# Kernel tuning notes

Measured on AMD Instinct MI355X. Metric: run time of the kernel, lower is better.

Reference implementation:

```python
import jax, jax.numpy as jnp
import numpy as np

IMAGE_SIZE = 256
DET = int(IMAGE_SIZE * 2 ** 0.5 + 0.5)  # 362 detector bins (diagonal coverage)
US = 4
N_ACQ = 45                     # acquired views: 0,4,...,176 degrees
N_FULL = (N_ACQ - 1) * US + 1  # 177 full (upsampled) views


def setup_inputs() -> dict:
    key = jax.random.key(0)
    k1, k2 = jax.random.split(key)
    x_source = jax.random.normal(k1, (2, 1, IMAGE_SIZE, IMAGE_SIZE), jnp.float32)
    s_target = jax.random.normal(k2, (2, 1, DET, N_ACQ), jnp.float32)
    theta_acq = np.arange(0, 180, 4, dtype=np.float64)  # 45 acquired angles
    segs = [np.linspace(theta_acq[i], theta_acq[i + 1], US + 1)[:-1] for i in range(N_ACQ - 1)]
    theta_full = np.concatenate(segs + [theta_acq[-1:]]).astype(np.float32)  # [177]
    acq_idx = (np.arange(N_ACQ) * US).astype(np.int32)  # positions of acquired angles in theta_full
    return {"x_source": x_source, "s_target": s_target,
            "thetas_deg": jnp.asarray(theta_full), "acq_idx": jnp.asarray(acq_idx)}


def bilinear_gather(img, xs, ys):
    # img: [B,C,H,W]; xs, ys: pixel coords [A,det,det]; zero outside the image.
    H, W = img.shape[-2], img.shape[-1]
    x0 = jnp.floor(xs); y0 = jnp.floor(ys)
    wx = xs - x0; wy = ys - y0
    x0i = x0.astype(jnp.int32); y0i = y0.astype(jnp.int32)

    def get(yi, xi):
        valid = (xi >= 0) & (xi < W) & (yi >= 0) & (yi < H)
        v = img[:, :, jnp.clip(yi, 0, H - 1), jnp.clip(xi, 0, W - 1)]  # [B,C,A,det,det]
        return jnp.where(valid, v, 0.0)

    return (get(y0i, x0i) * (1 - wy) * (1 - wx)
            + get(y0i, x0i + 1) * (1 - wy) * wx
            + get(y0i + 1, x0i) * wy * (1 - wx)
            + get(y0i + 1, x0i + 1) * wy * wx)


def radon(x, thetas_rad, det):
    # Ray-sum projection: sino[theta, t] = sum_s image(t*cos - s*sin, t*sin + s*cos)
    B, C, H, W = x.shape
    t = jnp.arange(det, dtype=x.dtype) - (det - 1) / 2.0  # centered detector/ray coord
    cos = jnp.cos(thetas_rad)[:, None, None]
    sin = jnp.sin(thetas_rad)[:, None, None]
    T = t[None, :, None]; S = t[None, None, :]
    xs = T * cos - S * sin + (W - 1) / 2.0  # [A,det,det]
    ys = T * sin + S * cos + (H - 1) / 2.0
    return bilinear_gather(x, xs, ys).sum(-1)  # [B,C,A,det]


def ramp_filter(size):
    # skimage/pytorch_radon style ramp built from its real-space kernel
    n = np.concatenate([np.arange(1, size // 2 + 1, 2), np.arange(size // 2 - 1, 0, -2)])
    f = np.zeros(size)
    f[0] = 0.25
    f[1::2] = -1.0 / (np.pi * n) ** 2
    return jnp.asarray(2 * np.real(np.fft.fft(f)), dtype=jnp.float32)


def fbp(sino, thetas_rad, image_size):
    # Filtered back-projection. sino: [B,C,det,A]
    B, C, det, A = sino.shape
    pad = max(64, int(2 ** np.ceil(np.log2(2 * det))))
    filt = ramp_filter(pad)  # [pad]
    sp = jnp.pad(sino, ((0, 0), (0, 0), (0, pad - det), (0, 0)))
    sf = jnp.fft.ifft(jnp.fft.fft(sp, axis=2) * filt[None, None, :, None], axis=2).real
    sf = jnp.transpose(sf[:, :, :det, :], (0, 1, 3, 2)).astype(sino.dtype)  # [B,C,A,det]
    g = jnp.arange(image_size, dtype=sino.dtype) - (image_size - 1) / 2.0
    cos = jnp.cos(thetas_rad); sin = jnp.sin(thetas_rad)
    # detector coordinate hit by each pixel, per angle: t = x*cos + y*sin
    t = (cos[:, None, None] * g[None, None, :]
         + sin[:, None, None] * g[None, :, None] + (det - 1) / 2.0)  # [A,H,W]
    t = t.reshape(A, -1)
    t0 = jnp.floor(t)
    w = t - t0
    t0i = t0.astype(jnp.int32)
    aidx = jnp.arange(A)[:, None]

    def samp(ti):
        valid = (ti >= 0) & (ti < det)
        return jnp.where(valid, sf[:, :, aidx, jnp.clip(ti, 0, det - 1)], 0.0)  # [B,C,A,HW]

    v = samp(t0i) * (1 - w) + samp(t0i + 1) * w
    reco = v.sum(2) * (jnp.pi / (2 * A))
    return reco.reshape(B, C, image_size, image_size)


def reference(x_source, s_target, thetas_deg, acq_idx):
    th = thetas_deg * (jnp.pi / 180.0)
    s = radon(x_source, th, DET)          # [B,C,A,det]
    s = jnp.transpose(s, (0, 1, 3, 2))    # [B,C,det,A] -- angle axis last, as in the module
    # masked data-consistency update: acquired columns become (target - predicted)
    s = s.at[..., acq_idx].set(s_target - s[..., acq_idx])
    return fbp(s, th, IMAGE_SIZE)
```

## Files before the change

kernel.cpp:

```cpp
#include <hip/hip_runtime.h>
#include <math.h>

#define IMG   256
#define NFULL 177
#define DETN  362
#define NACQ  45
#define PAD   1024

#define SINO_OFF 0
#define SF_OFF   131072
#define SEL_OFF  128160
#define PIMG_OFF 262144
#define PIMG_W   264
#define PIMG_N   (PIMG_W * PIMG_W)

#define TTILE  32
#define HALF_T 180.5f
#define TILE_N 5112

__constant__ const int kByOrder[12] = {5, 6, 4, 7, 3, 8, 2, 9, 1, 10, 0, 11};

__device__ __forceinline__ void gload16(const float* g, float* l) {
    __builtin_amdgcn_global_load_lds(
        (const __attribute__((address_space(1))) void*)g,
        (__attribute__((address_space(3))) void*)l, 16, 0, 0);
}

__global__ __launch_bounds__(256) void prep_kernel(
    const float* __restrict__ x, const float* __restrict__ thetas,
    float* __restrict__ pimg, int* __restrict__ sel, int padded)
{
    const int tid = threadIdx.x;

    if (padded) {
        const int i = blockIdx.x * 256 + tid;
        const int half = PIMG_W * (PIMG_W / 4);
        if (i < 2 * half) {
            const int b  = (i >= half) ? 1 : 0;
            const int j  = i - b * half;
            const int py = j / (PIMG_W / 4);
            const int px = (j - py * (PIMG_W / 4)) << 2;
            float4 v = make_float4(0.f, 0.f, 0.f, 0.f);
            if (py >= 4 && py < 260 && px >= 4 && px <= 256) {
                v = *(const float4*)(x + b * IMG * IMG + (py - 4) * IMG + (px - 4));
            }
            *(float4*)(pimg + b * PIMG_N + py * PIMG_W + px) = v;
        }
    }

    __shared__ int   hist[96];
    __shared__ float cs[2];
    const int a = blockIdx.x;
    if (tid < 96) hist[tid] = 0;
    if (tid == 0) {
        const float th = thetas[a] * (float)(M_PI / 180.0);
        cs[0] = cosf(th); cs[1] = sinf(th);
    }
    __syncthreads();
    const float c = cs[0], s = cs[1];
    if (tid < 64) {
        const int tt = tid >> 3, ts = tid & 7;
        #pragma unroll
        for (int p = 0; p < 3; ++p) {
            const float P  = 68.f + 4.f * (float)p;
            const float dT = s * P + c;
            const float dS = c * P - s;
            const int bank = (int)floorf((float)tt * dT + (float)ts * dS + 0.5f) & 31;
            atomicAdd(&hist[p * 32 + bank], 1);
        }
    }
    __syncthreads();
    if (tid == 0) {
        const float ac  = fabsf(c), as = fabsf(s);
        const float spx = 31.f * ac + 63.f * as;
        const float spy = 31.f * as + 63.f * ac;
        const int   hm[3] = {75, 71, 67};
        int best = 5, bcost = 1 << 30;
        for (int p = 0; p < 3; ++p) {
            int m = 0;
            for (int k = 0; k < 32; ++k) m = max(m, hist[p * 32 + k]);
            const float Pf = 68.f + 4.f * (float)p;
            const bool fit64 = (spx <= Pf - 8.05f) && (spy <= (float)hm[p] - 5.05f);
            if (fit64) { const int cst = 2 * m;     if (cst < bcost) { bcost = cst; best = p; } }
            {            const int cst = 2 * m + 3; if (cst < bcost) { bcost = cst; best = p + 3; } }
        }
        sel[a] = best;
    }
}

template<int P, int L>
__device__ __forceinline__ float radon_core(
    const float* __restrict__ img,
    const float* __restrict__ pimgb,
    float* tile, const int padded,
    const float c, const float s,
    const float xbase, const float ybase,
    const float xAB_mn, const float xAB_mx,
    const float yAB_mn, const float yAB_mx,
    const int SloB, const int ShiB, const int tid)
{
    constexpr int W4   = P / 4;
    constexpr int HMAX = TILE_N / P;
    const int ts   = tid & 7;
    const int wid  = tid >> 6;
    const int lane = tid & 63;
    float val = 0.0f;

    for (int Sseg = SloB; Sseg < ShiB; Sseg += L) {
        const float sv0 = (float)Sseg - HALF_T;
        const float sv1 = sv0 + (float)(L - 1);
        const float xmn = xAB_mn - sv1 * s;
        const float ya  = sv0 * c, yb = sv1 * c;
        const float ymn = yAB_mn + fminf(ya, yb);
        const float ymx = yAB_mx + fmaxf(ya, yb);
        const int ix0  = (int)floorf(xmn) - 1;
        const int iy0  = (int)floorf(ymn) - 1;
        const int ix0a = ix0 & ~3;
        const int h    = min((int)floorf(ymx) + 3 - iy0, HMAX);
        const int total4 = W4 * h;

        if (padded) {
            const int bx = ix0a + 4, by = iy0 + 4;
            const int nfull = total4 & ~63;
            for (int f0 = wid * 64; f0 < nfull; f0 += 256) {
                const int f  = f0 + lane;
                const int r  = f / W4;
                const int c4 = f - r * W4;
                const int px = min(max(bx + (c4 << 2), 0), PIMG_W - 4);
                const int py = min(max(by + r, 0), PIMG_W - 1);
                gload16(pimgb + py * PIMG_W + px, tile + (f0 << 2));
            }
            const int f = nfull + tid;
            if (f < total4) {
                const int r  = f / W4;
                const int c4 = f - r * W4;
                const int px = min(max(bx + (c4 << 2), 0), PIMG_W - 4);
                const int py = min(max(by + r, 0), PIMG_W - 1);
                *(float4*)(tile + (f << 2)) =
                    *(const float4*)(pimgb + py * PIMG_W + px);
            }
        } else {
            for (int f = tid; f < total4; f += 256) {
                const int r  = f / W4;
                const int c4 = f - r * W4;
                const int gy = iy0 + r;
                const int gx = ix0a + (c4 << 2);
                const int cyc = min(max(gy, 0), IMG - 1);
                const int cxc = min(max(gx, 0), IMG - 4);
                float4 v = *(const float4*)(img + cyc * IMG + cxc);
                const bool ok = ((unsigned)gy < (unsigned)IMG) &
                                ((unsigned)gx <= (unsigned)(IMG - 4));
                if (!ok) v = make_float4(0.f, 0.f, 0.f, 0.f);
                *(float4*)(tile + (f << 2)) = v;
            }
        }
        __syncthreads();

        const float xoff = xbase - (float)ix0a;
        const float yoff = ybase - (float)iy0;
        const int Send = min(Sseg + L, ShiB);

        auto samp = [&](float sval) {
            const float xs  = fmaf(-sval, s, xoff);
            const float ys  = fmaf(sval, c, yoff);
            const float x0f = floorf(xs);
            const float y0f = floorf(ys);
            const float wx  = xs - x0f;
            const float wy  = ys - y0f;
            const int base = (int)fmaf(y0f, (float)P, x0f);
            const float v00 = tile[base];
            const float v01 = tile[base + 1];
            const float v10 = tile[base + P];
            const float v11 = tile[base + P + 1];
            const float h0 = fmaf(wx, v01 - v00, v00);
            const float h1 = fmaf(wx, v11 - v10, v10);
            val += fmaf(wy, h1 - h0, h0);
        };

        if (Send - Sseg == L) {
            const float s0 = (float)(Sseg + ts) - HALF_T;
            #pragma unroll 4
            for (int u = 0; u < L / 8; ++u) samp(s0 + (float)(8 * u));
        } else {
            for (int S = Sseg + ts; S < Send; S += 8) samp((float)S - HALF_T);
        }
        __syncthreads();
    }
    return val;
}

__global__ __launch_bounds__(256, 8) void radon_kernel(
    const float* __restrict__ x, const float* __restrict__ pimg,
    const int* __restrict__ sel, const float* __restrict__ thetas,
    float* __restrict__ sino, int padded)
{
    const int blk = blockIdx.x;
    const int b = blk / NFULL;
    const int a = blk - b * NFULL;
    const int T0 = kByOrder[blockIdx.y] * TTILE;
    const int tid = threadIdx.x;
    const int ts = tid & 7;
    const int tt = tid >> 3;
    const int T = T0 + tt;

    __shared__ __align__(16) float tile[TILE_N];
    __shared__ int sRange[2];

    const float th = thetas[a] * (float)(M_PI / 180.0);
    const float c = cosf(th);
    const float s = sinf(th);
    const float cx = (IMG - 1) * 0.5f;
    const float cy = (IMG - 1) * 0.5f;
    const float Tc = (float)T - HALF_T;
    const float xbase = Tc * c + cx;
    const float ybase = Tc * s + cy;

    float lo = -1e30f, hi = 1e30f;
    bool empty = (T >= DETN);
    {   const float aa = -s;
        if (aa > 1e-5f)       { lo = fmaxf(lo, (-1.0f - xbase) / aa); hi = fminf(hi, (256.0f - xbase) / aa); }
        else if (aa < -1e-5f) { lo = fmaxf(lo, (256.0f - xbase) / aa); hi = fminf(hi, (-1.0f - xbase) / aa); }
        else if (xbase <= -1.0f || xbase >= 256.0f) empty = true;
    }
    {   const float aa = c;
        if (aa > 1e-5f)       { lo = fmaxf(lo, (-1.0f - ybase) / aa); hi = fminf(hi, (256.0f - ybase) / aa); }
        else if (aa < -1e-5f) { lo = fmaxf(lo, (256.0f - ybase) / aa); hi = fminf(hi, (-1.0f - ybase) / aa); }
        else if (ybase <= -1.0f || ybase >= 256.0f) empty = true;
    }
    lo = fmaxf(lo, -200.0f);
    hi = fminf(hi, 200.0f);
    int Slo = max(0, (int)floorf(lo + HALF_T) - 1);
    int Shi = min(DETN, (int)floorf(hi + HALF_T) + 2);
    if (empty || Shi < Slo) { Slo = 0; Shi = 0; }

    if (tid == 0) { sRange[0] = DETN; sRange[1] = 0; }
    __syncthreads();
    if (Shi > Slo) { atomicMin(&sRange[0], Slo); atomicMax(&sRange[1], Shi); }
    __syncthreads();
    const int SloB = sRange[0], ShiB = sRange[1];

    const float TcA = (float)T0 - HALF_T;
    const float TcB = (float)(T0 + TTILE - 1) - HALF_T;
    const float xAB_mn = fminf(TcA * c + cx, TcB * c + cx);
    const float xAB_mx = fmaxf(TcA * c + cx, TcB * c + cx);
    const float yAB_mn = fminf(TcA * s + cy, TcB * s + cy);
    const float yAB_mx = fmaxf(TcA * s + cy, TcB * s + cy);

    const float* __restrict__ img   = x + b * IMG * IMG;
    const float* __restrict__ pimgb = pimg + b * PIMG_N;
    const int selv = sel[a];

    float val;
    switch (selv) {
    case 0:  val = radon_core<68,64>(img, pimgb, tile, padded, c, s, xbase, ybase,
                                     xAB_mn, xAB_mx, yAB_mn, yAB_mx, SloB, ShiB, tid); break;
    case 1:  val = radon_core<72,64>(img, pimgb, tile, padded, c, s, xbase, ybase,
                                     xAB_mn, xAB_mx, yAB_mn, yAB_mx, SloB, ShiB, tid); break;
    case 2:  val = radon_core<76,64>(img, pimgb, tile, padded, c, s, xbase, ybase,
                                     xAB_mn, xAB_mx, yAB_mn, yAB_mx, SloB, ShiB, tid); break;
    case 3:  val = radon_core<68,48>(img, pimgb, tile, padded, c, s, xbase, ybase,
                                     xAB_mn, xAB_mx, yAB_mn, yAB_mx, SloB, ShiB, tid); break;
    case 4:  val = radon_core<72,48>(img, pimgb, tile, padded, c, s, xbase, ybase,
                                     xAB_mn, xAB_mx, yAB_mn, yAB_mx, SloB, ShiB, tid); break;
    default: val = radon_core<76,48>(img, pimgb, tile, padded, c, s, xbase, ybase,
                                     xAB_mn, xAB_mx, yAB_mn, yAB_mx, SloB, ShiB, tid); break;
    }

    val += __shfl_xor(val, 1, 8);
    val += __shfl_xor(val, 2, 8);
    val += __shfl_xor(val, 4, 8);
    if (ts == 0 && T < DETN) {
        sino[(b * NFULL + a) * DETN + T] = val;
    }
}

__global__ __launch_bounds__(192) void dc_filter_kernel(
    const float* __restrict__ sino,
    const float* __restrict__ st,
    const int*   __restrict__ acq,
    float* __restrict__ sf)
{
    const int blk = blockIdx.x;
    const int b = blk / NFULL;
    const int a = blk - b * NFULL;
    const int tid = threadIdx.x;

    __shared__ float col[DETN];
    __shared__ float gf[PAD];

    const float SC = (float)(M_PI / (2.0 * NFULL));
    const float c0 = 0.5f * SC;
    for (int n = tid; n < PAD; n += 192) {
        float v = 0.0f;
        if (n & 1) {
            const int d = (n < PAD - n) ? n : (PAD - n);
            const float pd = (float)M_PI * (float)d;
            v = -2.0f / (pd * pd) * SC;
        }
        gf[n] = v;
    }

    int inv = -1;
    for (int i = 0; i < NACQ; ++i) {
        if (acq[i] == a) inv = i;
    }

    for (int m = tid; m < DETN; m += 192) {
        float val = sino[(b * NFULL + a) * DETN + m];
        if (inv >= 0) {
            val = st[(b * DETN + m) * NACQ + inv] - val;
        }
        col[m] = val;
    }
    __syncthreads();

    const int T = blockIdx.y * 181 + tid;
    if (tid < 181) {
        const int m0 = (T + 1) & 1;
        float acc = c0 * col[T];
        #pragma unroll 4
        for (int k = 0; k < 181; ++k) {
            const int m = m0 + 2 * k;
            acc += col[m] * gf[(T - m) & (PAD - 1)];
        }
        sf[(b * NFULL + a) * DETN + T] = acc;
    }
}

__global__ __launch_bounds__(256) void backproject_kernel(
    const float* __restrict__ sf,
    const float* __restrict__ thetas,
    float* __restrict__ out)
{
    __shared__ float cb[2 * NFULL];
    __shared__ float red[256];
    const int tid = threadIdx.x;
    const int lane  = tid & 63;
    const int phase = tid >> 6;
    const int pix = blockIdx.x * 64 + lane;
    const int b = pix >> 16;
    const int y = (pix >> 8) & 255;
    const int xq = pix & 255;
    const float gx = (float)xq - (IMG - 1) * 0.5f;
    const float gy = (float)y  - (IMG - 1) * 0.5f;

    for (int a = tid; a < NFULL; a += 256) {
        float th = thetas[a] * (float)(M_PI / 180.0);
        cb[2 * a]     = cosf(th);
        cb[2 * a + 1] = fmaf(sinf(th), gy, HALF_T);
    }
    __syncthreads();

    const float* __restrict__ sfb = sf + b * NFULL * DETN;

    float acc = 0.0f;
    #pragma unroll 4
    for (int a = phase; a < NFULL; a += 4) {
        const float cs = cb[2 * a];
        const float bs = cb[2 * a + 1];
        const float t = fmaf(cs, gx, bs);
        const float t0f = floorf(t);
        const float w = t - t0f;
        const float* row = sfb + a * DETN + (int)t0f;
        const float v0 = row[0];
        const float v1 = row[1];
        acc += v0 + w * (v1 - v0);
    }
    red[tid] = acc;
    __syncthreads();
    if (tid < 64) {
        out[blockIdx.x * 64 + tid] =
            red[tid] + red[tid + 64] + red[tid + 128] + red[tid + 192];
    }
}

extern "C" void kernel_launch(void* const* d_in, const int* in_sizes, int n_in,
                              void* d_out, int out_size, void* d_ws, size_t ws_size,
                              hipStream_t stream) {
    const float* x      = (const float*)d_in[0];
    const float* st     = (const float*)d_in[1];
    const float* thetas = (const float*)d_in[2];
    const int*   acq    = (const int*)d_in[3];
    float* out  = (float*)d_out;
    float* wsf  = (float*)d_ws;
    float* sino = wsf + SINO_OFF;
    float* sf   = wsf + SF_OFF;
    int*   sel  = (int*)(wsf + SEL_OFF);
    float* pimg = wsf + PIMG_OFF;

    const size_t need = (size_t)(PIMG_OFF + 2 * PIMG_N) * sizeof(float);
    const int padded = (ws_size >= need) ? 1 : 0;

    prep_kernel<<<NFULL, 256, 0, stream>>>(x, thetas, pimg, sel, padded);
    dim3 gA(2 * NFULL, 12);
    radon_kernel<<<gA, 256, 0, stream>>>(x, pimg, sel, thetas, sino, padded);
    dim3 gB(2 * NFULL, 2);
    dc_filter_kernel<<<gB, 192, 0, stream>>>(sino, st, acq, sf);
    backproject_kernel<<<(2 * IMG * IMG) / 64, 256, 0, stream>>>(sf, thetas, out);
}
```

Baseline: 127.6 us.

## Remove prep kernel: fuse tile-pitch selection into radon and load directly from image

Drops the separate prep kernel that zero-padded the image and computed per-angle tile-pitch selection. The pitch selection is now computed inside each radon block with wave ballots and shuffles instead of an LDS histogram. Tile loads read the unpadded image directly, using async global-to-LDS loads when the whole wave is in bounds and a masked fallback otherwise. This saves a kernel launch and the padded-image traffic. In exchange, every block repeats the selection work and border wavefronts take a slower divergent path.

```diff
diff --git a/kernel.cpp b/kernel.cpp
--- a/kernel.cpp
+++ b/kernel.cpp
@@ -9,10 +9,6 @@
 
 #define SINO_OFF 0
 #define SF_OFF   131072
-#define SEL_OFF  128160
-#define PIMG_OFF 262144
-#define PIMG_W   264
-#define PIMG_N   (PIMG_W * PIMG_W)
 
 #define TTILE  32
 #define HALF_T 180.5f
@@ -26,77 +22,13 @@
         (__attribute__((address_space(3))) void*)l, 16, 0, 0);
 }
 
-__global__ __launch_bounds__(256) void prep_kernel(
-    const float* __restrict__ x, const float* __restrict__ thetas,
-    float* __restrict__ pimg, int* __restrict__ sel, int padded)
-{
-    const int tid = threadIdx.x;
-
-    if (padded) {
-        const int i = blockIdx.x * 256 + tid;
-        const int half = PIMG_W * (PIMG_W / 4);
-        if (i < 2 * half) {
-            const int b  = (i >= half) ? 1 : 0;
-            const int j  = i - b * half;
-            const int py = j / (PIMG_W / 4);
-            const int px = (j - py * (PIMG_W / 4)) << 2;
-            float4 v = make_float4(0.f, 0.f, 0.f, 0.f);
-            if (py >= 4 && py < 260 && px >= 4 && px <= 256) {
-                v = *(const float4*)(x + b * IMG * IMG + (py - 4) * IMG + (px - 4));
-            }
-            *(float4*)(pimg + b * PIMG_N + py * PIMG_W + px) = v;
-        }
-    }
-
-    __shared__ int   hist[96];
-    __shared__ float cs[2];
-    const int a = blockIdx.x;
-    if (tid < 96) hist[tid] = 0;
-    if (tid == 0) {
-        const float th = thetas[a] * (float)(M_PI / 180.0);
-        cs[0] = cosf(th); cs[1] = sinf(th);
-    }
-    __syncthreads();
-    const float c = cs[0], s = cs[1];
-    if (tid < 64) {
-        const int tt = tid >> 3, ts = tid & 7;
-        #pragma unroll
-        for (int p = 0; p < 3; ++p) {
-            const float P  = 68.f + 4.f * (float)p;
-            const float dT = s * P + c;
-            const float dS = c * P - s;
-            const int bank = (int)floorf((float)tt * dT + (float)ts * dS + 0.5f) & 31;
-            atomicAdd(&hist[p * 32 + bank], 1);
-        }
-    }
-    __syncthreads();
-    if (tid == 0) {
-        const float ac  = fabsf(c), as = fabsf(s);
-        const float spx = 31.f * ac + 63.f * as;
-        const float spy = 31.f * as + 63.f * ac;
-        const int   hm[3] = {75, 71, 67};
-        int best = 5, bcost = 1 << 30;
-        for (int p = 0; p < 3; ++p) {
-            int m = 0;
-            for (int k = 0; k < 32; ++k) m = max(m, hist[p * 32 + k]);
-            const float Pf = 68.f + 4.f * (float)p;
-            const bool fit64 = (spx <= Pf - 8.05f) && (spy <= (float)hm[p] - 5.05f);
-            if (fit64) { const int cst = 2 * m;     if (cst < bcost) { bcost = cst; best = p; } }
-            {            const int cst = 2 * m + 3; if (cst < bcost) { bcost = cst; best = p + 3; } }
-        }
-        sel[a] = best;
-    }
-}
-
 template<int P, int L>
 __device__ __forceinline__ float radon_core(
     const float* __restrict__ img,
-    const float* __restrict__ pimgb,
-    float* tile, const int padded,
+    float* tile,
     const float c, const float s,
     const float xbase, const float ybase,
-    const float xAB_mn, const float xAB_mx,
-    const float yAB_mn, const float yAB_mx,
+    const float xAB_mn, const float yAB_mn, const float yAB_mx,
     const int SloB, const int ShiB, const int tid)
 {
     constexpr int W4   = P / 4;
@@ -119,38 +51,34 @@
         const int h    = min((int)floorf(ymx) + 3 - iy0, HMAX);
         const int total4 = W4 * h;
 
-        if (padded) {
-            const int bx = ix0a + 4, by = iy0 + 4;
-            const int nfull = total4 & ~63;
-            for (int f0 = wid * 64; f0 < nfull; f0 += 256) {
-                const int f  = f0 + lane;
-                const int r  = f / W4;
-                const int c4 = f - r * W4;
-                const int px = min(max(bx + (c4 << 2), 0), PIMG_W - 4);
-                const int py = min(max(by + r, 0), PIMG_W - 1);
-                gload16(pimgb + py * PIMG_W + px, tile + (f0 << 2));
+        const int nfull = total4 & ~63;
+        for (int f0 = wid * 64; f0 < nfull; f0 += 256) {
+            const int f  = f0 + lane;
+            const int r  = f / W4;
+            const int c4 = f - r * W4;
+            const int gy = iy0 + r;
+            const int gx = ix0a + (c4 << 2);
+            const bool ok = ((unsigned)gy < (unsigned)IMG) &
+                            ((unsigned)gx <= (unsigned)(IMG - 4));
+            if (__all(ok)) {
+                gload16(img + gy * IMG + gx, tile + (f0 << 2));
+            } else {
+                float4 v = make_float4(0.f, 0.f, 0.f, 0.f);
+                if (ok) v = *(const float4*)(img + gy * IMG + gx);
+                *(float4*)(tile + (f << 2)) = v;
             }
+        }
+        {
             const int f = nfull + tid;
             if (f < total4) {
                 const int r  = f / W4;
                 const int c4 = f - r * W4;
-                const int px = min(max(bx + (c4 << 2), 0), PIMG_W - 4);
-                const int py = min(max(by + r, 0), PIMG_W - 1);
-                *(float4*)(tile + (f << 2)) =
-                    *(const float4*)(pimgb + py * PIMG_W + px);
-            }
-        } else {
-            for (int f = tid; f < total4; f += 256) {
-                const int r  = f / W4;
-                const int c4 = f - r * W4;
                 const int gy = iy0 + r;
                 const int gx = ix0a + (c4 << 2);
-                const int cyc = min(max(gy, 0), IMG - 1);
-                const int cxc = min(max(gx, 0), IMG - 4);
-                float4 v = *(const float4*)(img + cyc * IMG + cxc);
                 const bool ok = ((unsigned)gy < (unsigned)IMG) &
                                 ((unsigned)gx <= (unsigned)(IMG - 4));
-                if (!ok) v = make_float4(0.f, 0.f, 0.f, 0.f);
+                float4 v = make_float4(0.f, 0.f, 0.f, 0.f);
+                if (ok) v = *(const float4*)(img + gy * IMG + gx);
                 *(float4*)(tile + (f << 2)) = v;
             }
         }
@@ -190,9 +118,9 @@
 }
 
 __global__ __launch_bounds__(256, 8) void radon_kernel(
-    const float* __restrict__ x, const float* __restrict__ pimg,
-    const int* __restrict__ sel, const float* __restrict__ thetas,
-    float* __restrict__ sino, int padded)
+    const float* __restrict__ x,
+    const float* __restrict__ thetas,
+    float* __restrict__ sino)
 {
     const int blk = blockIdx.x;
     const int b = blk / NFULL;
@@ -205,6 +133,7 @@
 
     __shared__ __align__(16) float tile[TILE_N];
     __shared__ int sRange[2];
+    __shared__ int sSel;
 
     const float th = thetas[a] * (float)(M_PI / 180.0);
     const float c = cosf(th);
@@ -236,34 +165,62 @@
     if (tid == 0) { sRange[0] = DETN; sRange[1] = 0; }
     __syncthreads();
     if (Shi > Slo) { atomicMin(&sRange[0], Slo); atomicMax(&sRange[1], Shi); }
+
+    if (tid < 64) {
+        const int ltt = tid >> 3, lts = tid & 7;
+        const float ac = fabsf(c), as = fabsf(s);
+        const float spx = 31.f * ac + 63.f * as;
+        const float spy = 31.f * as + 63.f * ac;
+        const int hm[3] = {75, 71, 67};
+        int best = 5, bcost = 1 << 30;
+        #pragma unroll
+        for (int p = 0; p < 3; ++p) {
+            const float Pf = 68.f + 4.f * (float)p;
+            const float dT = s * Pf + c;
+            const float dS = c * Pf - s;
+            const int bank = (int)floorf((float)ltt * dT + (float)lts * dS + 0.5f) & 31;
+            unsigned long long m = ~0ull;
+            #pragma unroll
+            for (int bit = 0; bit < 5; ++bit) {
+                const unsigned long long bb = __ballot((bank >> bit) & 1);
+                m &= ((bank >> bit) & 1) ? bb : ~bb;
+            }
+            int cnt = __popcll(m);
+            #pragma unroll
+            for (int d = 1; d < 64; d <<= 1) cnt = max(cnt, __shfl_xor(cnt, d, 64));
+            if (spx <= Pf - 8.05f && spy <= (float)hm[p] - 5.05f) {
+                if (2 * cnt < bcost) { bcost = 2 * cnt; best = p; }
+            }
+            if (2 * cnt + 3 < bcost) { bcost = 2 * cnt + 3; best = p + 3; }
+        }
+        if (tid == 0) sSel = best;
+    }
     __syncthreads();
     const int SloB = sRange[0], ShiB = sRange[1];
+    const int selv = sSel;
 
     const float TcA = (float)T0 - HALF_T;
     const float TcB = (float)(T0 + TTILE - 1) - HALF_T;
     const float xAB_mn = fminf(TcA * c + cx, TcB * c + cx);
-    const float xAB_mx = fmaxf(TcA * c + cx, TcB * c + cx);
     const float yAB_mn = fminf(TcA * s + cy, TcB * s + cy);
     const float yAB_mx = fmaxf(TcA * s + cy, TcB * s + cy);
 
-    const float* __restrict__ img   = x + b * IMG * IMG;
-    const float* __restrict__ pimgb = pimg + b * PIMG_N;
-    const int selv = sel[a];
+    const float* __restrict__ img = x + b * IMG * IMG;
 
     float val;
     switch (selv) {
-    case 0:  val = radon_core<68,64>(img, pimgb, tile, padded, c, s, xbase, ybase,
-                                     xAB_mn, xAB_mx, yAB_mn, yAB_mx, SloB, ShiB, tid); break;
-    case 1:  val = radon_core<72,64>(img, pimgb, tile, padded, c, s, xbase, ybase,
-                                     xAB_mn, xAB_mx, yAB_mn, yAB_mx, SloB, ShiB, tid); break;
-    case 2:  val = radon_core<76,64>(img, pimgb, tile, padded, c, s, xbase, ybase,
-                                     xAB_mn, xAB_mx, yAB_mn, yAB_mx, SloB, ShiB, tid); break;
-    case 3:  val = radon_core<68,48>(img, pimgb, tile, padded, c, s, xbase, ybase,
-                                     xAB_mn, xAB_mx, yAB_mn, yAB_mx, SloB, ShiB, tid); break;
-    case 4:  val = radon_core<72,48>(img, pimgb, tile, padded, c, s, xbase, ybase,
-                                     xAB_mn, xAB_mx, yAB_mn, yAB_mx, SloB, ShiB, tid); break;
-    default: val = radon_core<76,48>(img, pimgb, tile, padded, c, s, xbase, ybase,
-                                     xAB_mn, xAB_mx, yAB_mn, yAB_mx, SloB, ShiB, tid); break;
+    case 0:  val = radon_core<68,64>(img, tile, c, s, xbase, ybase,
+                                     xAB_mn, yAB_mn, yAB_mx, SloB, ShiB, tid); break;
+    case 1:  val = radon_core<72,64>(img, tile, c, s, xbase, ybase,
+                                     xAB_mn, yAB_mn, yAB_mx, SloB, ShiB, tid); break;
+    case 2:  val = radon_core<76,64>(img, tile, c, s, xbase, ybase,
+                                     xAB_mn, yAB_mn, yAB_mx, SloB, ShiB, tid); break;
+    case 3:  val = radon_core<68,48>(img, tile, c, s, xbase, ybase,
+                                     xAB_mn, yAB_mn, yAB_mx, SloB, ShiB, tid); break;
+    case 4:  val = radon_core<72,48>(img, tile, c, s, xbase, ybase,
+                                     xAB_mn, yAB_mn, yAB_mx, SloB, ShiB, tid); break;
+    default: val = radon_core<76,48>(img, tile, c, s, xbase, ybase,
+                                     xAB_mn, yAB_mn, yAB_mx, SloB, ShiB, tid); break;
     }
 
     val += __shfl_xor(val, 1, 8);
@@ -385,15 +342,9 @@
     float* wsf  = (float*)d_ws;
     float* sino = wsf + SINO_OFF;
     float* sf   = wsf + SF_OFF;
-    int*   sel  = (int*)(wsf + SEL_OFF);
-    float* pimg = wsf + PIMG_OFF;
-
-    const size_t need = (size_t)(PIMG_OFF + 2 * PIMG_N) * sizeof(float);
-    const int padded = (ws_size >= need) ? 1 : 0;
-
-    prep_kernel<<<NFULL, 256, 0, stream>>>(x, thetas, pimg, sel, padded);
+
     dim3 gA(2 * NFULL, 12);
-    radon_kernel<<<gA, 256, 0, stream>>>(x, pimg, sel, thetas, sino, padded);
+    radon_kernel<<<gA, 256, 0, stream>>>(x, thetas, sino);
     dim3 gB(2 * NFULL, 2);
     dc_filter_kernel<<<gB, 192, 0, stream>>>(sino, st, acq, sf);
     backproject_kernel<<<(2 * IMG * IMG) / 64, 256, 0, stream>>>(sf, thetas, out);
```

New measurement: 128.0 us. About the same (+0.3%).
